# Kernel optimization log

Measured on AMD Instinct MI355X. Metric: run time of the kernel, lower is better.

Reference implementation:

```python
import jax, jax.numpy as jnp
import numpy as np

B = 2
IMG = (128, 256, 256)
P = 16
E, NH, DH = 768, 12, 64
L, F = 12, 3072
WS = (512, 1024, 2048)   # LongNet segment lengths
RS = (1, 2, 4)           # matching dilation ratios
NEG = -1e9
NPATCH = (IMG[0] // P) * (IMG[1] // P) * (IMG[2] // P)
S = NPATCH + 1           # +1 CLS token


def setup_inputs() -> dict:
    key = jax.random.key(0)
    ks = jax.random.split(key, 16)
    def nrm(k, shape, std=0.02):
        return jax.random.normal(k, shape, jnp.float32) * std
    return {
        "x": jax.random.normal(ks[0], (B, 1) + IMG, jnp.float32),
        "conv_w": nrm(ks[1], (E, 1, P, P, P)),
        "conv_b": jnp.zeros((E,), jnp.float32),
        "cls_token": nrm(ks[2], (1, 1, E)),
        "pos_embed": nrm(ks[3], (1, S, E)),
        "ln1_g": jnp.ones((L, E)), "ln1_b": jnp.zeros((L, E)),
        "wq": nrm(ks[4], (L, E, E)), "bq": jnp.zeros((L, E)),
        "wk": nrm(ks[5], (L, E, E)), "bk": jnp.zeros((L, E)),
        "wv": nrm(ks[6], (L, E, E)), "bv": jnp.zeros((L, E)),
        "wo": nrm(ks[7], (L, E, E)), "bo": jnp.zeros((L, E)),
        "ln2_g": jnp.ones((L, E)), "ln2_b": jnp.zeros((L, E)),
        "w1": nrm(ks[8], (L, E, F)), "b1": jnp.zeros((L, F)),
        "w2": nrm(ks[9], (L, F, E)), "b2": jnp.zeros((L, E)),
        "normf_g": jnp.ones((E,)), "normf_b": jnp.zeros((E,)),
    }


def _ln(x, g, b, eps=1e-5):
    m = x.mean(-1, keepdims=True)
    v = ((x - m) ** 2).mean(-1, keepdims=True)
    return (x - m) * jax.lax.rsqrt(v + eps) * g + b


def _dilated_branch(q, k, v, w, r):
    # LongNet dilated attention for one (segment_length w, dilation r) config.
    # q,k,v: [B,S,H,d]. Head h uses offset h % r inside each segment of length w.
    b, s0, h, d = q.shape
    sp = -(-s0 // w) * w
    pad = sp - s0
    qp, kp, vp = (jnp.pad(t, ((0, 0), (0, pad), (0, 0), (0, 0))) for t in (q, k, v))
    n, m = sp // w, w // r
    idx = (jnp.arange(h)[:, None] % r) + jnp.arange(m)[None, :] * r      # [h,m]
    seg = lambda t: t.reshape(b, n, w, h, d).transpose(0, 1, 3, 2, 4)    # [b,n,h,w,d]
    gidx = idx[None, None, :, :, None]
    qs = jnp.take_along_axis(seg(qp), gidx, axis=3)                      # [b,n,h,m,d]
    ks = jnp.take_along_axis(seg(kp), gidx, axis=3)
    vs = jnp.take_along_axis(seg(vp), gidx, axis=3)
    kvalid = (jnp.arange(sp) < s0).reshape(n, w)[:, idx]                 # [n,h,m]
    scores = jnp.einsum('bnhqd,bnhkd->bnhqk', qs, ks) * (d ** -0.5)
    scores = jnp.where(kvalid[None, :, :, None, :], scores, NEG)
    lse = jax.nn.logsumexp(scores, axis=-1)                              # [b,n,h,m]
    out = jnp.einsum('bnhqk,bnhkd->bnhqd', jax.nn.softmax(scores, -1), vs)
    hh = jnp.arange(h)[:, None]
    out_f = jnp.zeros((b, n, h, w, d), q.dtype).at[:, :, hh, idx, :].set(out)
    lse_f = jnp.full((b, n, h, w), NEG, q.dtype).at[:, :, hh, idx].set(lse)
    return (out_f.transpose(0, 1, 3, 2, 4).reshape(b, sp, h, d),
            lse_f.transpose(0, 1, 3, 2).reshape(b, sp, h))


def _dilated_attention(q, k, v):
    # Combine branches weighted by softmax normalizers (exp lse), per LongNet.
    b, s0, h, d = q.shape
    smax = max(-(-s0 // w) * w for w in WS)
    outs, lses = [], []
    for w, r in zip(WS, RS):
        o, l = _dilated_branch(q, k, v, w, r)
        outs.append(jnp.pad(o, ((0, 0), (0, smax - o.shape[1]), (0, 0), (0, 0))))
        lses.append(jnp.pad(l, ((0, 0), (0, smax - l.shape[1]), (0, 0)),
                            constant_values=NEG))
    wgt = jax.nn.softmax(jnp.stack(lses), axis=0)[..., None]             # [nb,b,smax,h,1]
    out = (wgt * jnp.stack(outs)).sum(0)                                 # [b,smax,h,d]
    return out[:, :s0]


def reference(x, conv_w, conv_b, cls_token, pos_embed, ln1_g, ln1_b, wq, bq,
              wk, bk, wv, bv, wo, bo, ln2_g, ln2_b, w1, b1, w2, b2,
              normf_g, normf_b):
    b = x.shape[0]
    dp, hp, wp = IMG[0] // P, IMG[1] // P, IMG[2] // P
    # Conv3d patch embed with stride == kernel -> block reshape + matmul
    xp = x.reshape(b, 1, dp, P, hp, P, wp, P).transpose(0, 2, 4, 6, 1, 3, 5, 7)
    xp = xp.reshape(b, dp * hp * wp, -1) @ conv_w.reshape(E, -1).T + conv_b
    h = jnp.concatenate([jnp.broadcast_to(cls_token, (b, 1, E)), xp], axis=1)
    h = h + pos_embed  # seq length matches pos_embed, no interpolation needed

    def layer(hst, p):
        g1, lb1, Wq, Bq, Wk, Bk, Wv, Bv, Wo, Bo, g2, lb2, W1, B1, W2, B2 = p
        y = _ln(hst, g1, lb1)
        q = (y @ Wq + Bq).reshape(b, S, NH, DH)
        k = (y @ Wk + Bk).reshape(b, S, NH, DH)
        v = (y @ Wv + Bv).reshape(b, S, NH, DH)
        a = _dilated_attention(q, k, v).reshape(b, S, E) @ Wo + Bo
        hst = hst + a
        y = _ln(hst, g2, lb2)
        hst = hst + jax.nn.gelu(y @ W1 + B1, approximate=False) @ W2 + B2
        return hst, None

    params = (ln1_g, ln1_b, wq, bq, wk, bk, wv, bv, wo, bo,
              ln2_g, ln2_b, w1, b1, w2, b2)
    h, _ = jax.lax.scan(layer, h, params)
    h = _ln(h, normf_g, normf_b)
    return h[:, 0]
```

## Files before the change

### kernel.cpp

```cpp
#include <hip/hip_runtime.h>
#include <math.h>

#define SEQ 2049
#define EMB 768
#define NHEADS 12
#define QKVW 2304
#define MROWS 4098
#define MPAD 4224
#define NEGV -1000000000.0f

typedef short bs8 __attribute__((ext_vector_type(8)));
typedef float f4 __attribute__((ext_vector_type(4)));

__device__ __forceinline__ unsigned short f2bf(float f){
  union { float f; unsigned u; } x; x.f = f;
  unsigned r = x.u + 0x7fffu + ((x.u >> 16) & 1u);
  return (unsigned short)(r >> 16);
}
__device__ __forceinline__ float bf2f(unsigned short u){
  union { unsigned u; float f; } x; x.u = ((unsigned)u) << 16; return x.f;
}

__device__ __forceinline__ float gelu_f(float x){
  float ax = fabsf(x)*0.70710678f;
  float t = 1.f/(1.f + 0.3275911f*ax);
  float p = t*(0.254829592f + t*(-0.284496736f + t*(1.421413741f
            + t*(-1.453152027f + t*1.061405429f))));
  float erfv = 1.f - p*__expf(-ax*ax);
  float s = (x >= 0.f) ? erfv : -erfv;
  return 0.5f*x*(1.f + s);
}

__device__ __forceinline__ void gl_lds16(const void* g, void* l){
  __builtin_amdgcn_global_load_lds((const __attribute__((address_space(1))) void*)g,
                                   (__attribute__((address_space(3))) void*)l, 16, 0, 0);
}

__global__ void wtr_k(const float* __restrict__ src, unsigned short* __restrict__ dst,
                      int K, int N, int LD, int NOFF)
{
  __shared__ float tile[32][33];
  int k0 = blockIdx.x*32, n0 = blockIdx.y*32, z = blockIdx.z;
  int tx = threadIdx.x, ty = threadIdx.y;
  const float* s = src + (size_t)z*K*N;
#pragma unroll
  for (int i=0;i<4;++i)
    tile[ty*4+i][tx] = s[(size_t)(k0+ty*4+i)*N + n0+tx];
  __syncthreads();
  unsigned short* dz = dst + ((size_t)z*LD + NOFF)*K;
#pragma unroll
  for (int i=0;i<4;++i)
    dz[(size_t)(n0+ty*4+i)*K + k0+tx] = f2bf(tile[tx][ty*4+i]);
}

__global__ void castconv_k(const float* __restrict__ src, unsigned short* __restrict__ dst){
  size_t i = ((size_t)blockIdx.x*256 + threadIdx.x)*4;
  float4 f = *(const float4*)(src+i);
  dst[i+0]=f2bf(f.x); dst[i+1]=f2bf(f.y); dst[i+2]=f2bf(f.z); dst[i+3]=f2bf(f.w);
}

__global__ void biascat_k(const float* __restrict__ bq, const float* __restrict__ bk,
                          const float* __restrict__ bv, float* __restrict__ dst){
  int i = blockIdx.x*256+threadIdx.x;
  int l = i/QKVW, c = i%QKVW;
  float v = (c<768) ? bq[l*768+c] : (c<1536 ? bk[l*768+c-768] : bv[l*768+c-1536]);
  dst[i] = v;
}

__global__ void patchify_k(const float* __restrict__ x, unsigned short* __restrict__ Xp)
{
  size_t gid = (size_t)blockIdx.x*256 + threadIdx.x;
  size_t oi = gid*4;
  int row = (int)(oi >> 12);
  int c = (int)(oi & 4095);
  int b = row >> 11; int p = row & 2047;
  int pd = p >> 8, ph = (p>>4)&15, pw = p&15;
  int pz = c >> 8, py = (c>>4)&15, px = c&15;
  size_t src = (((size_t)(b*128 + pd*16+pz)*256) + (size_t)(ph*16+py))*256 + (size_t)(pw*16+px);
  float4 f = *(const float4*)(x+src);
  Xp[oi+0]=f2bf(f.x); Xp[oi+1]=f2bf(f.y); Xp[oi+2]=f2bf(f.z); Xp[oi+3]=f2bf(f.w);
}

__global__ void assemble_k(const float* __restrict__ P, size_t pstride,
                           const float* __restrict__ cls,
                           const float* __restrict__ pos_e, float* __restrict__ H)
{
  int row = blockIdx.x; int t = threadIdx.x;
  float* hr = H + (size_t)row*EMB;
  if (row >= MROWS) { hr[t]=0.f; hr[t+256]=0.f; hr[t+512]=0.f; return; }
  int b = row / SEQ; int pos = row - b*SEQ;
#pragma unroll
  for (int c0=0;c0<3;++c0) {
    int c = t + c0*256;
    float v;
    if (pos==0) v = cls[c];
    else {
      size_t idx = ((size_t)(b*2048 + pos-1))*EMB + c;
      v = P[idx] + P[pstride+idx] + P[2*pstride+idx] + P[3*pstride+idx];
    }
    hr[c] = v + pos_e[(size_t)pos*EMB + c];
  }
}

__global__ __launch_bounds__(256) void ln_k(const float* __restrict__ H,
    const float* __restrict__ gam, const float* __restrict__ bet,
    unsigned short* __restrict__ Y)
{
  int row = blockIdx.x, t = threadIdx.x;
  const float* hr = H + (size_t)row*EMB;
  float v0 = hr[t], v1 = hr[t+256], v2 = hr[t+512];
  float s = v0+v1+v2;
#pragma unroll
  for (int off=32; off>=1; off>>=1) s += __shfl_down(s, off);
  __shared__ float r1[4], r2[4];
  if ((t&63)==0) r1[t>>6] = s;
  __syncthreads();
  float mean = (r1[0]+r1[1]+r1[2]+r1[3]) * (1.f/768.f);
  float d0=v0-mean, d1=v1-mean, d2=v2-mean;
  float q = d0*d0+d1*d1+d2*d2;
#pragma unroll
  for (int off=32; off>=1; off>>=1) q += __shfl_down(q, off);
  if ((t&63)==0) r2[t>>6] = q;
  __syncthreads();
  float rstd = rsqrtf((r2[0]+r2[1]+r2[2]+r2[3])*(1.f/768.f) + 1e-5f);
  unsigned short* yr = Y + (size_t)row*EMB;
  yr[t]     = f2bf(d0*rstd*gam[t]     + bet[t]);
  yr[t+256] = f2bf(d1*rstd*gam[t+256] + bet[t+256]);
  yr[t+512] = f2bf(d2*rstd*gam[t+512] + bet[t+512]);
}

template<int S>
__global__ __launch_bounds__(256) void ln_red_k(float* __restrict__ H,
    const float* __restrict__ P, size_t pstride,
    const float* __restrict__ gam, const float* __restrict__ bet,
    unsigned short* __restrict__ Y)
{
  int row = blockIdx.x, t = threadIdx.x;
  size_t base = (size_t)row*EMB;
  float v[3];
#pragma unroll
  for (int c0=0;c0<3;++c0) {
    size_t idx = base + t + c0*256;
    float h = H[idx];
#pragma unroll
    for (int s=0;s<S;++s) h += P[(size_t)s*pstride + idx];
    H[idx] = h; v[c0] = h;
  }
  float s = v[0]+v[1]+v[2];
#pragma unroll
  for (int off=32; off>=1; off>>=1) s += __shfl_down(s, off);
  __shared__ float r1[4], r2[4];
  if ((t&63)==0) r1[t>>6] = s;
  __syncthreads();
  float mean = (r1[0]+r1[1]+r1[2]+r1[3]) * (1.f/768.f);
  float d0=v[0]-mean, d1=v[1]-mean, d2=v[2]-mean;
  float q = d0*d0+d1*d1+d2*d2;
#pragma unroll
  for (int off=32; off>=1; off>>=1) q += __shfl_down(q, off);
  if ((t&63)==0) r2[t>>6] = q;
  __syncthreads();
  float rstd = rsqrtf((r2[0]+r2[1]+r2[2]+r2[3])*(1.f/768.f) + 1e-5f);
  unsigned short* yr = Y + base;
  yr[t]     = f2bf(d0*rstd*gam[t]     + bet[t]);
  yr[t+256] = f2bf(d1*rstd*gam[t+256] + bet[t+256]);
  yr[t+512] = f2bf(d2*rstd*gam[t+512] + bet[t+512]);
}

__global__ __launch_bounds__(256) void final_ln_red_k(const float* __restrict__ H,
   const float* __restrict__ P, size_t pstride,
   const float* __restrict__ gam, const float* __restrict__ bet, float* __restrict__ out)
{
  int b = blockIdx.x, t = threadIdx.x;
  size_t base = (size_t)(b*SEQ)*EMB;
  float v[3];
#pragma unroll
  for (int c0=0;c0<3;++c0) {
    size_t idx = base + t + c0*256;
    float h = H[idx];
#pragma unroll
    for (int s=0;s<4;++s) h += P[(size_t)s*pstride + idx];
    v[c0] = h;
  }
  float s = v[0]+v[1]+v[2];
#pragma unroll
  for (int off=32; off>=1; off>>=1) s += __shfl_down(s, off);
  __shared__ float r1[4], r2[4];
  if ((t&63)==0) r1[t>>6] = s;
  __syncthreads();
  float mean = (r1[0]+r1[1]+r1[2]+r1[3]) * (1.f/768.f);
  float d0=v[0]-mean, d1=v[1]-mean, d2=v[2]-mean;
  float q = d0*d0+d1*d1+d2*d2;
#pragma unroll
  for (int off=32; off>=1; off>>=1) q += __shfl_down(q, off);
  if ((t&63)==0) r2[t>>6] = q;
  __syncthreads();
  float rstd = rsqrtf((r2[0]+r2[1]+r2[2]+r2[3])*(1.f/768.f) + 1e-5f);
  out[b*EMB + t]     = d0*rstd*gam[t]     + bet[t];
  out[b*EMB + t+256] = d1*rstd*gam[t+256] + bet[t+256];
  out[b*EMB + t+512] = d2*rstd*gam[t+512] + bet[t+512];
}

template<int MODE, int NSPLIT>
__global__ __launch_bounds__(256) void gemm_k(
    const unsigned short* __restrict__ A,
    const unsigned short* __restrict__ Bt,
    const float* __restrict__ bias,
    unsigned short* __restrict__ Cb,
    float* __restrict__ Cf,
    int K, int ldc, size_t splitStride)
{
  __shared__ __attribute__((aligned(16))) unsigned short lA[3][128*32];
  __shared__ __attribute__((aligned(16))) unsigned short lB[3][128*32];
  const int tid = threadIdx.x;
  const int w = tid>>6, lane = tid&63, g = lane>>4, l16 = lane&15;
  const int lr = lane>>2;
  const int lcs = (((lane&3) ^ ((lane>>3)&3)))*8;
  const int swz = ((g ^ ((l16>>1)&3)))*8;
  const int nwg = gridDim.x*gridDim.y;
  const int id = blockIdx.y*gridDim.x + blockIdx.x;
  const int q = nwg>>3, r = nwg&7, xc = id&7, si = id>>3;
  const int nid = (xc<r ? xc*(q+1) : r*(q+1)+(xc-r)*q) + si;
  const int tm = nid / gridDim.x;
  const int tn = nid - tm*gridDim.x;
  const int kchunk = K / NSPLIT;
  const int kofs = (NSPLIT>1) ? blockIdx.z * kchunk : 0;
  const unsigned short* Ab = A + (size_t)tm*128*K + kofs;
  const unsigned short* Bb = Bt + (size_t)tn*128*K + kofs;
  const int wm = (w>>1)*64, wn = (w&1)*64;
  f4 acc[4][4] = {};
  const int nkt = kchunk>>5;

  auto STAGE = [&](int buf, int kt){
    const size_t ko = (size_t)(kt*32 + lcs);
    gl_lds16(Ab + (size_t)(w*16 + lr)*K + ko,     ((char*)lA[buf]) + w*1024);
    gl_lds16(Ab + (size_t)((w+4)*16 + lr)*K + ko, ((char*)lA[buf]) + (w+4)*1024);
    gl_lds16(Bb + (size_t)(w*16 + lr)*K + ko,     ((char*)lB[buf]) + w*1024);
    gl_lds16(Bb + (size_t)((w+4)*16 + lr)*K + ko, ((char*)lB[buf]) + (w+4)*1024);
  };

  STAGE(0, 0);
  STAGE(1, 1);
  for (int kt=0; kt<nkt; ++kt) {
    const int cur = kt % 3;
    if (kt+2 < nkt) {
      STAGE((kt+2)%3, kt+2);
      asm volatile("s_waitcnt vmcnt(8)" ::: "memory");
    } else if (kt+1 < nkt) {
      asm volatile("s_waitcnt vmcnt(4)" ::: "memory");
    } else {
      asm volatile("s_waitcnt vmcnt(0)" ::: "memory");
    }
    __builtin_amdgcn_sched_barrier(0);
    __builtin_amdgcn_s_barrier();
    bs8 af[4], bf[4];
#pragma unroll
    for (int mi=0;mi<4;++mi) af[mi] = *(const bs8*)(lA[cur] + (wm+mi*16+l16)*32 + swz);
#pragma unroll
    for (int ni=0;ni<4;++ni) bf[ni] = *(const bs8*)(lB[cur] + (wn+ni*16+l16)*32 + swz);
    asm volatile("s_waitcnt lgkmcnt(0)" ::: "memory");
    __builtin_amdgcn_sched_barrier(0);
    __builtin_amdgcn_s_barrier();
#pragma unroll
    for (int mi=0;mi<4;++mi)
#pragma unroll
      for (int ni=0;ni<4;++ni)
        acc[mi][ni] = __builtin_amdgcn_mfma_f32_16x16x32_bf16(af[mi], bf[ni], acc[mi][ni], 0,0,0);
  }
  const float bscale = (NSPLIT==1 || blockIdx.z==0) ? 1.f : 0.f;
#pragma unroll
  for (int mi=0;mi<4;++mi)
#pragma unroll
    for (int ni=0;ni<4;++ni) {
      int col = tn*128 + wn + ni*16 + l16;
      float bv = bias[col]*bscale;
#pragma unroll
      for (int r0=0;r0<4;++r0) {
        int row = tm*128 + wm + mi*16 + g*4 + r0;
        float val = acc[mi][ni][r0] + bv;
        if (MODE==1) val = gelu_f(val);
        if (MODE<=1) Cb[(size_t)row*ldc + col] = f2bf(val);
        else Cf[(size_t)blockIdx.z*splitStride + (size_t)row*ldc + col] = val;
      }
    }
}

__global__ __launch_bounds__(256) void attn_all_k(
    const unsigned short* __restrict__ qkv,
    unsigned short* __restrict__ O1, float* __restrict__ L1,
    unsigned short* __restrict__ O2, float* __restrict__ L2,
    unsigned short* __restrict__ O3, float* __restrict__ L3)
{
  __shared__ __attribute__((aligned(16))) unsigned short lK[128*72];
  __shared__ __attribute__((aligned(16))) unsigned short lVt[64*136];
  __shared__ __attribute__((aligned(16))) unsigned short Pl[4][16][136];
  const int tid = threadIdx.x;
  const int w = tid>>6, lane = tid&63, g = lane>>4, l16 = lane&15;

  int id = blockIdx.x;
  int R, WSZ, NSEG; unsigned short* OB; float* LB;
  if (id < 960)       { R=1; WSZ=512;  NSEG=5; OB=O1; LB=L1; }
  else if (id < 1536) { id -= 960;  R=2; WSZ=1024; NSEG=3; OB=O2; LB=L2; }
  else                { id -= 1536; R=4; WSZ=2048; NSEG=2; OB=O3; LB=L3; }
  const int qt = id & 7; int rest = id >> 3;
  const int seg = rest % NSEG; const int bh = rest / NSEG;
  const int b = bh / NHEADS, hd = bh % NHEADS;
  const int hr = hd % R;
  const int j0 = qt*64 + w*16;
  const int kbase = seg*WSZ + hr;
  const unsigned short* qkvb = qkv + (size_t)b*SEQ*QKVW;

  bs8 z = {0,0,0,0,0,0,0,0};
  bs8 qf0 = z, qf1 = z;
  {
    int qpos = kbase + (j0 + l16)*R;
    if (qpos < SEQ) {
      const unsigned short* qrow = qkvb + (size_t)qpos*QKVW + hd*64 + g*8;
      qf0 = *(const bs8*)(qrow);
      qf1 = *(const bs8*)(qrow + 32);
    }
  }

  float rm[4], rs[4];
  f4 oacc[4] = {};
#pragma unroll
  for (int r=0;r<4;++r) { rm[r] = NEGV; rs[r] = 0.f; }

  for (int c=0; c<4; ++c) {
    __syncthreads();
#pragma unroll
    for (int it=0; it<4; ++it) {
      int idx = tid + it*256;
      int kk = idx >> 3, dblk = idx & 7;
      int kpos = kbase + (c*128 + kk)*R;
      bs8 kv = z;
      if (kpos < SEQ) kv = *(const bs8*)(qkvb + (size_t)kpos*QKVW + EMB + hd*64 + dblk*8);
      *(bs8*)(lK + kk*72 + dblk*8) = kv;
    }
#pragma unroll
    for (int it=0; it<4; ++it) {
      int idx = tid + it*256;
      int kk = idx & 127, dblk = idx >> 7;
      int kpos = kbase + (c*128 + kk)*R;
      unsigned short tv[8] = {0,0,0,0,0,0,0,0};
      if (kpos < SEQ)
        *(bs8*)tv = *(const bs8*)(qkvb + (size_t)kpos*QKVW + 1536 + hd*64 + dblk*8);
#pragma unroll
      for (int ii=0; ii<8; ++ii) lVt[(dblk*8+ii)*136 + kk] = tv[ii];
    }
    __syncthreads();

    f4 sc[8];
#pragma unroll
    for (int kt=0; kt<8; ++kt) {
      int key = kt*16 + l16;
      bs8 kf0 = *(const bs8*)(lK + key*72 + g*8);
      bs8 kf1 = *(const bs8*)(lK + key*72 + 32 + g*8);
      f4 acc = {0.f,0.f,0.f,0.f};
      acc = __builtin_amdgcn_mfma_f32_16x16x32_bf16(qf0, kf0, acc, 0,0,0);
      acc = __builtin_amdgcn_mfma_f32_16x16x32_bf16(qf1, kf1, acc, 0,0,0);
      int kpos = kbase + (c*128 + key)*R;
      bool kvld = (kpos < SEQ);
#pragma unroll
      for (int r=0;r<4;++r) sc[kt][r] = kvld ? acc[r]*0.125f : NEGV;
    }
    float scl[4];
#pragma unroll
    for (int r=0;r<4;++r) {
      float mx = sc[0][r];
#pragma unroll
      for (int kt=1;kt<8;++kt) mx = fmaxf(mx, sc[kt][r]);
      mx = fmaxf(mx, __shfl_xor(mx, 1));
      mx = fmaxf(mx, __shfl_xor(mx, 2));
      mx = fmaxf(mx, __shfl_xor(mx, 4));
      mx = fmaxf(mx, __shfl_xor(mx, 8));
      float mn = fmaxf(rm[r], mx);
      scl[r] = __expf(rm[r] - mn);
      rm[r] = mn;
    }
#pragma unroll
    for (int r=0;r<4;++r) {
      float sm = 0.f;
#pragma unroll
      for (int kt=0;kt<8;++kt) { float p = __expf(sc[kt][r] - rm[r]); sc[kt][r] = p; sm += p; }
      sm += __shfl_xor(sm, 1); sm += __shfl_xor(sm, 2);
      sm += __shfl_xor(sm, 4); sm += __shfl_xor(sm, 8);
      rs[r] = rs[r]*scl[r] + sm;
    }
#pragma unroll
    for (int dt=0; dt<4; ++dt)
#pragma unroll
      for (int r=0;r<4;++r) oacc[dt][r] *= scl[r];
#pragma unroll
    for (int kt=0;kt<8;++kt)
#pragma unroll
      for (int r=0;r<4;++r)
        Pl[w][g*4+r][kt*16+l16] = f2bf(sc[kt][r]);
#pragma unroll
    for (int ks=0; ks<4; ++ks) {
      bs8 pa = *(const bs8*)(&Pl[w][l16][ks*32 + g*8]);
#pragma unroll
      for (int dt=0; dt<4; ++dt) {
        bs8 vb = *(const bs8*)(lVt + (dt*16+l16)*136 + ks*32 + g*8);
        oacc[dt] = __builtin_amdgcn_mfma_f32_16x16x32_bf16(pa, vb, oacc[dt], 0,0,0);
      }
    }
  }

  size_t obase = ((size_t)(b*NSEG + seg)*NHEADS + hd)*512;
#pragma unroll
  for (int dt=0; dt<4; ++dt)
#pragma unroll
    for (int r=0;r<4;++r) {
      int j = j0 + g*4 + r;
      OB[(obase + j)*64 + dt*16 + l16] = f2bf(oacc[dt][r] / rs[r]);
    }
  if (l16 == 0) {
#pragma unroll
    for (int r=0;r<4;++r) LB[obase + j0 + g*4 + r] = rm[r] + __logf(rs[r]);
  }
}

__global__ __launch_bounds__(256) void attn_combine_k(
   const unsigned short* __restrict__ o1, const float* __restrict__ l1,
   const unsigned short* __restrict__ o2, const float* __restrict__ l2,
   const unsigned short* __restrict__ o3, const float* __restrict__ l3,
   unsigned short* __restrict__ attn)
{
  int row = blockIdx.x; int t = threadIdx.x;
  unsigned short* arow = attn + (size_t)row*EMB;
  if (row >= MROWS) { arow[t]=0; arow[t+256]=0; arow[t+512]=0; return; }
  int b = row / SEQ, pos = row - (row/SEQ)*SEQ;
#pragma unroll
  for (int c0=0; c0<3; ++c0) {
    int cc = t + c0*256;
    int hd = cc >> 6, d = cc & 63;
    float L0,L1v,L2v,O0,O1v,O2v;
    {
      int seg = pos >> 9; int j = pos & 511;
      size_t base = ((size_t)(b*5 + seg)*NHEADS + hd)*512 + j;
      L0 = l1[base]; O0 = bf2f(o1[base*64 + d]);
    }
    if ((pos & 1) == (hd & 1)) {
      int seg = pos >> 10; int j = ((pos & 1023) - (hd&1)) >> 1;
      size_t base = ((size_t)(b*3 + seg)*NHEADS + hd)*512 + j;
      L1v = l2[base]; O1v = bf2f(o2[base*64 + d]);
    } else { L1v = NEGV; O1v = 0.f; }
    if ((pos & 3) == (hd & 3)) {
      int seg = pos >> 11; int j = ((pos & 2047) - (hd&3)) >> 2;
      size_t base = ((size_t)(b*2 + seg)*NHEADS + hd)*512 + j;
      L2v = l3[base]; O2v = bf2f(o3[base*64 + d]);
    } else { L2v = NEGV; O2v = 0.f; }
    float m = fmaxf(L0, fmaxf(L1v, L2v));
    float e0 = __expf(L0-m), e1 = __expf(L1v-m), e2 = __expf(L2v-m);
    float inv = 1.f/(e0+e1+e2);
    arow[cc] = f2bf((e0*O0+e1*O1v+e2*O2v)*inv);
  }
}

extern "C" void kernel_launch(void* const* d_in, const int* in_sizes, int n_in,
                              void* d_out, int out_size, void* d_ws, size_t ws_size,
                              hipStream_t stream) {
  const float* x       = (const float*)d_in[0];
  const float* conv_w  = (const float*)d_in[1];
  const float* conv_b  = (const float*)d_in[2];
  const float* cls     = (const float*)d_in[3];
  const float* pos_e   = (const float*)d_in[4];
  const float* ln1_g   = (const float*)d_in[5];
  const float* ln1_b   = (const float*)d_in[6];
  const float* wq      = (const float*)d_in[7];
  const float* bq      = (const float*)d_in[8];
  const float* wk      = (const float*)d_in[9];
  const float* bk      = (const float*)d_in[10];
  const float* wv      = (const float*)d_in[11];
  const float* bv      = (const float*)d_in[12];
  const float* wo      = (const float*)d_in[13];
  const float* bo      = (const float*)d_in[14];
  const float* ln2_g   = (const float*)d_in[15];
  const float* ln2_b   = (const float*)d_in[16];
  const float* w1      = (const float*)d_in[17];
  const float* b1      = (const float*)d_in[18];
  const float* w2      = (const float*)d_in[19];
  const float* b2      = (const float*)d_in[20];
  const float* nf_g    = (const float*)d_in[21];
  const float* nf_b    = (const float*)d_in[22];

  char* ws = (char*)d_ws;
  size_t off = 0;
  auto alloc = [&](size_t bytes)->char* {
    char* p = ws + off; off += (bytes + 255) & ~(size_t)255; return p;
  };
  unsigned short* wqkv_t = (unsigned short*)alloc((size_t)12*2304*768*2);
  unsigned short* wo_t   = (unsigned short*)alloc((size_t)12*768*768*2);
  unsigned short* w1_t   = (unsigned short*)alloc((size_t)12*3072*768*2);
  unsigned short* w2_t   = (unsigned short*)alloc((size_t)12*768*3072*2);
  unsigned short* cw_b   = (unsigned short*)alloc((size_t)768*4096*2);
  float* bqkv            = (float*)alloc((size_t)12*2304*4);
  unsigned short* Xp     = (unsigned short*)alloc((size_t)4096*4096*2);
  float* H               = (float*)alloc((size_t)MPAD*768*4);
  float* P               = (float*)alloc((size_t)4*MPAD*768*4);
  unsigned short* Y      = (unsigned short*)alloc((size_t)MPAD*768*2);
  unsigned short* QKV    = (unsigned short*)alloc((size_t)MPAD*2304*2);
  unsigned short* ATT    = (unsigned short*)alloc((size_t)MPAD*768*2);
  unsigned short* Y2     = (unsigned short*)alloc((size_t)MPAD*3072*2);
  unsigned short* O1 = (unsigned short*)alloc((size_t)2*5*12*512*64*2);
  unsigned short* O2 = (unsigned short*)alloc((size_t)2*3*12*512*64*2);
  unsigned short* O3 = (unsigned short*)alloc((size_t)2*2*12*512*64*2);
  float* L1 = (float*)alloc((size_t)2*5*12*512*4);
  float* L2 = (float*)alloc((size_t)2*3*12*512*4);
  float* L3 = (float*)alloc((size_t)2*2*12*512*4);
  const size_t PSTR = (size_t)MPAD*768;

  dim3 tb(32,8);
  wtr_k<<<dim3(24,24,12), tb, 0, stream>>>(wq, wqkv_t, 768, 768, 2304, 0);
  wtr_k<<<dim3(24,24,12), tb, 0, stream>>>(wk, wqkv_t, 768, 768, 2304, 768);
  wtr_k<<<dim3(24,24,12), tb, 0, stream>>>(wv, wqkv_t, 768, 768, 2304, 1536);
  wtr_k<<<dim3(24,24,12), tb, 0, stream>>>(wo, wo_t, 768, 768, 768, 0);
  wtr_k<<<dim3(24,96,12), tb, 0, stream>>>(w1, w1_t, 768, 3072, 3072, 0);
  wtr_k<<<dim3(96,24,12), tb, 0, stream>>>(w2, w2_t, 3072, 768, 768, 0);
  castconv_k<<<3072,256,0,stream>>>(conv_w, cw_b);
  biascat_k<<<108,256,0,stream>>>(bq,bk,bv,bqkv);
  patchify_k<<<16384,256,0,stream>>>(x, Xp);
  gemm_k<3,4><<<dim3(6,32,4),256,0,stream>>>(Xp, cw_b, conv_b, nullptr, P, 4096, 768, PSTR);
  assemble_k<<<MPAD,256,0,stream>>>(P, PSTR, cls, pos_e, H);

  for (int l=0;l<12;++l) {
    if (l==0) ln_k<<<MPAD,256,0,stream>>>(H, ln1_g, ln1_b, Y);
    else ln_red_k<4><<<MPAD,256,0,stream>>>(H, P, PSTR, ln1_g + l*768, ln1_b + l*768, Y);
    gemm_k<0,1><<<dim3(18,33),256,0,stream>>>(Y, wqkv_t + (size_t)l*2304*768, bqkv + l*2304, QKV, nullptr, 768, 2304, 0);
    attn_all_k<<<1920,256,0,stream>>>(QKV, O1,L1,O2,L2,O3,L3);
    attn_combine_k<<<MPAD,256,0,stream>>>(O1,L1,O2,L2,O3,L3, ATT);
    gemm_k<3,2><<<dim3(6,33,2),256,0,stream>>>(ATT, wo_t + (size_t)l*768*768, bo + l*768, nullptr, P, 768, 768, PSTR);
    ln_red_k<2><<<MPAD,256,0,stream>>>(H, P, PSTR, ln2_g + l*768, ln2_b + l*768, Y);
    gemm_k<1,1><<<dim3(24,33),256,0,stream>>>(Y, w1_t + (size_t)l*3072*768, b1 + l*3072, Y2, nullptr, 768, 3072, 0);
    gemm_k<3,4><<<dim3(6,33,4),256,0,stream>>>(Y2, w2_t + (size_t)l*768*3072, b2 + l*768, nullptr, P, 3072, 768, PSTR);
  }
  final_ln_red_k<<<2,256,0,stream>>>(H, P, PSTR, nf_g, nf_b, (float*)d_out);
}
```

Measured before the change: 3.020 ms.

## Prefetch K/V into registers, remap attention blocks, cheaper bf16 rounding, reduce split-K

The attention kernel now loads the next K/V chunk into registers while computing on the current one, replacing the synchronous load-then-compute loop with register double-buffering. Block indices are permuted so neighbouring blocks mix the three dilation branches, and the P-matrix bf16 conversion uses a simpler round-half-up. The FFN down-projection GEMM drops from 4-way to 2-way split-K, with the residual-reduction kernels adjusted to sum two partials. The costs are higher register pressure in attention, slightly different rounding, and less parallelism in the W2 GEMM.

```diff
diff --git a/kernel.cpp b/kernel.cpp
--- a/kernel.cpp
+++ b/kernel.cpp
@@ -16,6 +16,10 @@
   union { float f; unsigned u; } x; x.f = f;
   unsigned r = x.u + 0x7fffu + ((x.u >> 16) & 1u);
   return (unsigned short)(r >> 16);
+}
+__device__ __forceinline__ unsigned short f2bf_fast(float f){
+  union { float f; unsigned u; } x; x.f = f;
+  return (unsigned short)((x.u + 0x8000u) >> 16);
 }
 __device__ __forceinline__ float bf2f(unsigned short u){
   union { unsigned u; float f; } x; x.u = ((unsigned)u) << 16; return x.f;
@@ -166,6 +170,7 @@
   yr[t+512] = f2bf(d2*rstd*gam[t+512] + bet[t+512]);
 }
 
+template<int S>
 __global__ __launch_bounds__(256) void final_ln_red_k(const float* __restrict__ H,
    const float* __restrict__ P, size_t pstride,
    const float* __restrict__ gam, const float* __restrict__ bet, float* __restrict__ out)
@@ -178,7 +183,7 @@
     size_t idx = base + t + c0*256;
     float h = H[idx];
 #pragma unroll
-    for (int s=0;s<4;++s) h += P[(size_t)s*pstride + idx];
+    for (int s=0;s<S;++s) h += P[(size_t)s*pstride + idx];
     v[c0] = h;
   }
   float s = v[0]+v[1]+v[2];
@@ -296,7 +301,7 @@
   const int tid = threadIdx.x;
   const int w = tid>>6, lane = tid&63, g = lane>>4, l16 = lane&15;
 
-  int id = blockIdx.x;
+  int id = (blockIdx.x & 7)*240 + (blockIdx.x >> 3);
   int R, WSZ, NSEG; unsigned short* OB; float* LB;
   if (id < 960)       { R=1; WSZ=512;  NSEG=5; OB=O1; LB=L1; }
   else if (id < 1536) { id -= 960;  R=2; WSZ=1024; NSEG=3; OB=O2; LB=L2; }
@@ -320,34 +325,45 @@
     }
   }
 
+  bs8 kreg[4], vreg[4];
+  auto ISSUE = [&](int c){
+#pragma unroll
+    for (int it=0; it<4; ++it) {
+      int idx = tid + it*256;
+      int kkK = idx >> 3, dbK = idx & 7;
+      int kposK = kbase + (c*128 + kkK)*R;
+      bs8 kv = z;
+      if (kposK < SEQ) kv = *(const bs8*)(qkvb + (size_t)kposK*QKVW + EMB + hd*64 + dbK*8);
+      kreg[it] = kv;
+      int kkV = idx & 127, dbV = idx >> 7;
+      int kposV = kbase + (c*128 + kkV)*R;
+      bs8 vv = z;
+      if (kposV < SEQ) vv = *(const bs8*)(qkvb + (size_t)kposV*QKVW + 1536 + hd*64 + dbV*8);
+      vreg[it] = vv;
+    }
+  };
+
   float rm[4], rs[4];
   f4 oacc[4] = {};
 #pragma unroll
   for (int r=0;r<4;++r) { rm[r] = NEGV; rs[r] = 0.f; }
 
+  ISSUE(0);
   for (int c=0; c<4; ++c) {
-    __syncthreads();
+    __builtin_amdgcn_s_barrier();
 #pragma unroll
     for (int it=0; it<4; ++it) {
       int idx = tid + it*256;
-      int kk = idx >> 3, dblk = idx & 7;
-      int kpos = kbase + (c*128 + kk)*R;
-      bs8 kv = z;
-      if (kpos < SEQ) kv = *(const bs8*)(qkvb + (size_t)kpos*QKVW + EMB + hd*64 + dblk*8);
-      *(bs8*)(lK + kk*72 + dblk*8) = kv;
-    }
-#pragma unroll
-    for (int it=0; it<4; ++it) {
-      int idx = tid + it*256;
-      int kk = idx & 127, dblk = idx >> 7;
-      int kpos = kbase + (c*128 + kk)*R;
-      unsigned short tv[8] = {0,0,0,0,0,0,0,0};
-      if (kpos < SEQ)
-        *(bs8*)tv = *(const bs8*)(qkvb + (size_t)kpos*QKVW + 1536 + hd*64 + dblk*8);
-#pragma unroll
-      for (int ii=0; ii<8; ++ii) lVt[(dblk*8+ii)*136 + kk] = tv[ii];
-    }
-    __syncthreads();
+      int kkK = idx >> 3, dbK = idx & 7;
+      *(bs8*)(lK + kkK*72 + dbK*8) = kreg[it];
+      int kkV = idx & 127, dbV = idx >> 7;
+#pragma unroll
+      for (int ii=0; ii<8; ++ii) lVt[(dbV*8+ii)*136 + kkV] = (unsigned short)vreg[it][ii];
+    }
+    asm volatile("s_waitcnt lgkmcnt(0)" ::: "memory");
+    __builtin_amdgcn_sched_barrier(0);
+    __builtin_amdgcn_s_barrier();
+    if (c+1 < 4) ISSUE(c+1);
 
     f4 sc[8];
 #pragma unroll
@@ -394,7 +410,7 @@
     for (int kt=0;kt<8;++kt)
 #pragma unroll
       for (int r=0;r<4;++r)
-        Pl[w][g*4+r][kt*16+l16] = f2bf(sc[kt][r]);
+        Pl[w][g*4+r][kt*16+l16] = f2bf_fast(sc[kt][r]);
 #pragma unroll
     for (int ks=0; ks<4; ++ks) {
       bs8 pa = *(const bs8*)(&Pl[w][l16][ks*32 + g*8]);
@@ -525,14 +541,14 @@
 
   for (int l=0;l<12;++l) {
     if (l==0) ln_k<<<MPAD,256,0,stream>>>(H, ln1_g, ln1_b, Y);
-    else ln_red_k<4><<<MPAD,256,0,stream>>>(H, P, PSTR, ln1_g + l*768, ln1_b + l*768, Y);
+    else ln_red_k<2><<<MPAD,256,0,stream>>>(H, P, PSTR, ln1_g + l*768, ln1_b + l*768, Y);
     gemm_k<0,1><<<dim3(18,33),256,0,stream>>>(Y, wqkv_t + (size_t)l*2304*768, bqkv + l*2304, QKV, nullptr, 768, 2304, 0);
     attn_all_k<<<1920,256,0,stream>>>(QKV, O1,L1,O2,L2,O3,L3);
     attn_combine_k<<<MPAD,256,0,stream>>>(O1,L1,O2,L2,O3,L3, ATT);
     gemm_k<3,2><<<dim3(6,33,2),256,0,stream>>>(ATT, wo_t + (size_t)l*768*768, bo + l*768, nullptr, P, 768, 768, PSTR);
     ln_red_k<2><<<MPAD,256,0,stream>>>(H, P, PSTR, ln2_g + l*768, ln2_b + l*768, Y);
     gemm_k<1,1><<<dim3(24,33),256,0,stream>>>(Y, w1_t + (size_t)l*3072*768, b1 + l*3072, Y2, nullptr, 768, 3072, 0);
-    gemm_k<3,4><<<dim3(6,33,4),256,0,stream>>>(Y2, w2_t + (size_t)l*768*3072, b2 + l*768, nullptr, P, 3072, 768, PSTR);
-  }
-  final_ln_red_k<<<2,256,0,stream>>>(H, P, PSTR, nf_g, nf_b, (float*)d_out);
-}
+    gemm_k<3,2><<<dim3(6,33,2),256,0,stream>>>(Y2, w2_t + (size_t)l*768*3072, b2 + l*768, nullptr, P, 3072, 768, PSTR);
+  }
+  final_ln_red_k<2><<<2,256,0,stream>>>(H, P, PSTR, nf_g, nf_b, (float*)d_out);
+}
```

Result: faster. 2.856 ms (-5.5%).
